# Optimization experiments

Measured on AMD Instinct MI355X. Metric: run time of the kernel, lower is better.

## Reference

```python
import jax, jax.numpy as jnp
import numpy as np

NUM_GROUPS = 5
EPS = 1e-5
QB = 128.0  # 2**(8-1) for b=8 activation quantization


def _binarize_weights_groupwise(W):
    """Sign-binarize W group-wise along out-feature dim, STE on backward.
    Faithful to torch: rows beyond num_groups*group_size remain zero."""
    n_out = W.shape[0]
    gs = n_out // NUM_GROUPS
    Wb = jnp.zeros_like(W)
    for g in range(NUM_GROUPS):  # small fixed loop (5 groups)
        wg = W[g * gs:(g + 1) * gs]
        z = wg - wg.mean()
        # STE: forward = sign(z), backward = identity w.r.t. z
        ste = z + jax.lax.stop_gradient(jnp.sign(z) - z)
        Wb = Wb.at[g * gs:(g + 1) * gs].set(ste)
    return Wb


def _quantize_activations_groupwise(x):
    """8-bit absmax quantization group-wise along dim 0 (batch), per torch code."""
    n = x.shape[0]
    gs = n // NUM_GROUPS
    xq = jnp.zeros_like(x)
    for g in range(NUM_GROUPS):
        ag = x[g * gs:(g + 1) * gs]
        gamma = jnp.max(jnp.abs(ag))
        xq = xq.at[g * gs:(g + 1) * gs].set(
            jnp.clip(ag * QB / (gamma + EPS), -QB + EPS, QB - EPS))
    return xq


def _bitlinear(x, W, b):
    Wb = _binarize_weights_groupwise(W)
    y = jnp.einsum('btc,oc->bto', x, Wb) + b
    return _quantize_activations_groupwise(y)


def setup_inputs() -> dict:
    key = jax.random.key(0)
    k1, k2, k3, k4, k5 = jax.random.split(key, 5)
    B, T, C = 10, 2048, 384
    H = 4 * C
    lim1 = 1.0 / np.sqrt(C)
    lim2 = 1.0 / np.sqrt(H)
    x = jax.random.normal(k1, (B, T, C), dtype=jnp.float32)
    W1 = jax.random.uniform(k2, (H, C), minval=-lim1, maxval=lim1, dtype=jnp.float32)
    b1 = jax.random.uniform(k3, (H,), minval=-lim1, maxval=lim1, dtype=jnp.float32)
    W2 = jax.random.uniform(k4, (C, H), minval=-lim2, maxval=lim2, dtype=jnp.float32)
    b2 = jax.random.uniform(k5, (C,), minval=-lim2, maxval=lim2, dtype=jnp.float32)
    return {"x": x, "W1": W1, "b1": b1, "W2": W2, "b2": b2}


def reference(x, W1, b1, W2, b2):
    h = _bitlinear(x, W1, b1)           # [B,T,4C], quantized to [-128,128]
    h = jax.nn.gelu(h, approximate=False)  # torch nn.GELU default is exact
    out = _bitlinear(h, W2, b2)         # [B,T,C]
    return out  # nn.Dropout is identity in eval/reference mode
```

## Files before the change

kernel.cpp:

```cpp
#include <hip/hip_runtime.h>
#include <cstdint>
#include <cstddef>

#define THREADS 256
#define NB 8

typedef float f32x4 __attribute__((ext_vector_type(4)));
typedef __bf16 bf16x8 __attribute__((ext_vector_type(8)));
typedef __bf16 bf16x4 __attribute__((ext_vector_type(4)));

__device__ __forceinline__ void gload_lds16(const void* g, void* l) {
    auto gp = (const __attribute__((address_space(1))) unsigned int*)(unsigned long long)(uintptr_t)g;
    auto lp = (__attribute__((address_space(3))) unsigned int*)(unsigned int)(uintptr_t)l;
    __builtin_amdgcn_global_load_lds(gp, lp, 16, 0, 0);
}

__device__ __forceinline__ float gelu_fast(float f) {
    const float z = f * 0.70710678118654752f;
    const float az = fabsf(z);
    const float t = __builtin_amdgcn_rcpf(fmaf(0.3275911f, az, 1.0f));
    float poly = fmaf(1.061405429f, t, -1.453152027f);
    poly = fmaf(poly, t, 1.421413741f);
    poly = fmaf(poly, t, -0.284496736f);
    poly = fmaf(poly, t, 0.254829592f);
    poly *= t;
    const float e = __builtin_amdgcn_exp2f(-az * az * 1.44269504088896f);
    float erfv = fmaf(-poly, e, 1.0f);
    erfv = copysignf(erfv, z);
    return 0.5f * f * (1.0f + erfv);
}

__global__ void prep_a(const float* __restrict__ x, __bf16* __restrict__ xb,
                       const float* __restrict__ W1, const float* __restrict__ W2,
                       float* __restrict__ partials, int epg1, int epg2,
                       unsigned int* __restrict__ gzero) {
    const int blk = blockIdx.x, tid = threadIdx.x;
    if (blk < 80) {
        const int y = blk >> 3, b = blk & 7;
        if (blk == 0 && tid < 16) gzero[tid] = 0u;
        const int epg = (y < 5) ? epg1 : epg2;
        const float* Wg = (y < 5) ? (W1 + (size_t)y * epg1)
                                  : (W2 + (size_t)(y - 5) * epg2);
        const int chunk4 = epg / (4 * NB);
        const float* base = Wg + (size_t)b * chunk4 * 4;
        float s = 0.f;
        for (int i = tid; i < chunk4; i += THREADS) {
            f32x4 v = *reinterpret_cast<const f32x4*>(base + 4 * (size_t)i);
            s += (v[0] + v[1]) + (v[2] + v[3]);
        }
        __shared__ float red[THREADS];
        red[tid] = s;
        __syncthreads();
        for (int off = THREADS / 2; off > 0; off >>= 1) {
            if (tid < off) red[tid] += red[tid + off];
            __syncthreads();
        }
        if (tid == 0) partials[y * NB + b] = red[0];
        return;
    }
    const int i = (blk - 80) * THREADS + tid;
    f32x4 v = *reinterpret_cast<const f32x4*>(x + 4 * (size_t)i);
    bf16x4 o;
    o[0] = (__bf16)v[0]; o[1] = (__bf16)v[1];
    o[2] = (__bf16)v[2]; o[3] = (__bf16)v[3];
    *reinterpret_cast<bf16x4*>(xb + 4 * (size_t)i) = o;
}

__global__ void prep_b(const float* __restrict__ W1, __bf16* __restrict__ W1b,
                       const float* __restrict__ W2, __bf16* __restrict__ W2b,
                       const float* __restrict__ psums,
                       int epg1, int tail1, int epg2, int tail2) {
    int r = blockIdx.x;
    const int tid = threadIdx.x;
    const float* W; __bf16* Wb; const float* ps; int epg, tail;
    if (r <= 40) { W = W1; Wb = W1b; ps = psums;      epg = epg1; tail = tail1; }
    else { r -= 41; W = W2; Wb = W2b; ps = psums + 40; epg = epg2; tail = tail2; }
    if (r == 40) {
        __bf16* og = Wb + (size_t)5 * epg;
        for (int i = tid; i < tail; i += THREADS) og[i] = (__bf16)0.f;
        return;
    }
    const int g = r >> 3, b = r & 7;
    float total = 0.f;
#pragma unroll
    for (int j = 0; j < NB; ++j) total += ps[g * NB + j];
    const float mean = total / (float)epg;
    const int chunk4 = epg / (4 * NB);
    const size_t off0 = (size_t)g * epg + (size_t)b * chunk4 * 4;
    const float* base = W + off0;
    __bf16* ob = Wb + off0;
    for (int i = tid; i < chunk4; i += THREADS) {
        f32x4 v = *reinterpret_cast<const f32x4*>(base + 4 * (size_t)i);
        bf16x4 o;
#pragma unroll
        for (int j = 0; j < 4; ++j) {
            const float z = v[j] - mean;
            o[j] = (__bf16)((z > 0.f) ? 1.f : ((z < 0.f) ? -1.f : 0.f));
        }
        *reinterpret_cast<bf16x4*>(ob + 4 * (size_t)i) = o;
    }
}

template<int OUT_BF16>
__global__ __launch_bounds__(512, 1)
void gemm_p3(const __bf16* __restrict__ A, const __bf16* __restrict__ Bw,
             const float* __restrict__ bias, void* __restrict__ outp,
             unsigned int* __restrict__ gmax, int M, int N, int K,
             int GN, int nwg) {
    constexpr int BM = 256, BN_ = 128, BK = 64, NF = 2;
    constexpr int ABYTES = BM * BK * 2;
    constexpr int BBYTES = BN_ * BK * 2;
    constexpr int BUF = ABYTES + BBYTES;
    __shared__ __attribute__((aligned(16))) char lds[3 * BUF];

    const int tid = threadIdx.x;
    const int wave = tid >> 6, lane = tid & 63;
    const int l15 = lane & 15, l4 = lane >> 4;
    const int wr = wave >> 2, wc = wave & 3;

    const int cpx = nwg >> 3;
    const int orig = (blockIdx.x & 7) * cpx + (blockIdx.x >> 3);
    const int bm = orig / GN, bn = orig % GN;

    const __bf16* Ab = A + (size_t)bm * BM * K;
    const __bf16* Bb = Bw + (size_t)bn * BN_ * K;
    const int NT = K / BK;

    f32x4 acc[8][NF];
#pragma unroll
    for (int m = 0; m < 8; ++m)
#pragma unroll
        for (int n = 0; n < NF; ++n)
            acc[m][n] = f32x4{0.f, 0.f, 0.f, 0.f};

    auto STAGE = [&](int t, int buf) {
        const int k0 = t * BK;
        char* ab = lds + buf * BUF;
        char* bb = ab + ABYTES;
#pragma unroll
        for (int j = 0; j < 4; ++j) {
            const int q = j * 8192 + tid * 16;
            const int lr = q >> 7;
            const int s = ((q >> 4) & 7) ^ (lr & 7);
            gload_lds16(Ab + (size_t)lr * K + k0 + s * 8, ab + q);
        }
#pragma unroll
        for (int j = 0; j < 2; ++j) {
            const int q = j * 8192 + tid * 16;
            const int lr = q >> 7;
            const int s = ((q >> 4) & 7) ^ (lr & 7);
            gload_lds16(Bb + (size_t)lr * K + k0 + s * 8, bb + q);
        }
    };

    STAGE(0, 0);
    STAGE(1, 1);
    asm volatile("s_waitcnt vmcnt(6)" ::: "memory");
    __syncthreads();

    int cur = 0;
    for (int t = 0; t < NT; ++t) {
        const int nxt2 = (cur >= 1) ? cur - 1 : cur + 2;
        if (t + 2 < NT) STAGE(t + 2, nxt2);
        const char* ab = lds + cur * BUF;
        const char* bb = ab + ABYTES;
#pragma unroll
        for (int kk = 0; kk < 2; ++kk) {
            bf16x8 af[8], bfv[NF];
#pragma unroll
            for (int m = 0; m < 8; ++m) {
                const int r = wr * 128 + m * 16 + l15;
                const int sp = (kk * 4 + l4) ^ (r & 7);
                af[m] = *reinterpret_cast<const bf16x8*>(ab + r * 128 + sp * 16);
            }
#pragma unroll
            for (int n = 0; n < NF; ++n) {
                const int r = wc * 32 + n * 16 + l15;
                const int sp = (kk * 4 + l4) ^ (r & 7);
                bfv[n] = *reinterpret_cast<const bf16x8*>(bb + r * 128 + sp * 16);
            }
#pragma unroll
            for (int m = 0; m < 8; ++m)
#pragma unroll
                for (int n = 0; n < NF; ++n)
                    acc[m][n] = __builtin_amdgcn_mfma_f32_16x16x32_bf16(
                        bfv[n], af[m], acc[m][n], 0, 0, 0);
        }
        if (t + 2 < NT)      asm volatile("s_waitcnt vmcnt(6)" ::: "memory");
        else if (t + 1 < NT) asm volatile("s_waitcnt vmcnt(0)" ::: "memory");
        __syncthreads();
        cur = (cur == 2) ? 0 : cur + 1;
    }

    const int rowb = bm * BM + wr * 128;
    const int colb = bn * BN_ + wc * 32;
    float lmax = 0.f;
#pragma unroll
    for (int n = 0; n < NF; ++n) {
        const f32x4 bv = *reinterpret_cast<const f32x4*>(bias + colb + n * 16 + l4 * 4);
#pragma unroll
        for (int m = 0; m < 8; ++m) {
            const int row = rowb + m * 16 + l15;
            if (OUT_BF16) {
                bf16x4 o;
#pragma unroll
                for (int r = 0; r < 4; ++r) {
                    const float v = acc[m][n][r] + bv[r];
                    lmax = fmaxf(lmax, fabsf(v));
                    o[r] = (__bf16)v;
                }
                *reinterpret_cast<bf16x4*>(
                    &((__bf16*)outp)[(size_t)row * N + colb + n * 16 + l4 * 4]) = o;
            } else {
                f32x4 o;
#pragma unroll
                for (int r = 0; r < 4; ++r) {
                    o[r] = acc[m][n][r] + bv[r];
                    lmax = fmaxf(lmax, fabsf(o[r]));
                }
                *reinterpret_cast<f32x4*>(
                    &((float*)outp)[(size_t)row * N + colb + n * 16 + l4 * 4]) = o;
            }
        }
    }
#pragma unroll
    for (int off = 32; off > 0; off >>= 1)
        lmax = fmaxf(lmax, __shfl_down(lmax, off, 64));
    float* wredmax = (float*)lds;
    if (lane == 0) wredmax[wave] = lmax;
    __syncthreads();
    if (tid == 0) {
        float bmax = wredmax[0];
#pragma unroll
        for (int w = 1; w < 8; ++w) bmax = fmaxf(bmax, wredmax[w]);
        atomicMax(gmax + (bm * BM) / 4096, __float_as_uint(bmax));
    }
}

__global__ void quant_gelu(__bf16* __restrict__ y, const unsigned int* __restrict__ gbits,
                           int perg8, int n8) {
    const int stride = gridDim.x * blockDim.x;
    for (int i = blockIdx.x * blockDim.x + threadIdx.x; i < n8; i += stride) {
        const int g = i / perg8;
        const float gamma = __uint_as_float(gbits[g]);
        const float s = 128.0f / (gamma + 1e-5f);
        bf16x8 v = *reinterpret_cast<const bf16x8*>(y + 8 * (size_t)i);
        bf16x8 o;
#pragma unroll
        for (int j = 0; j < 8; ++j) {
            float f = (float)v[j] * s;
            f = fminf(fmaxf(f, -128.0f + 1e-5f), 128.0f - 1e-5f);
            o[j] = (__bf16)gelu_fast(f);
        }
        *reinterpret_cast<bf16x8*>(y + 8 * (size_t)i) = o;
    }
}

__global__ void final_scale(float* __restrict__ y, const unsigned int* __restrict__ gbits,
                            int perg4, int n4) {
    int i = blockIdx.x * blockDim.x + threadIdx.x;
    if (i >= n4) return;
    const int g = i / perg4;
    const float gamma = __uint_as_float(gbits[g]);
    const float s = 128.0f / (gamma + 1e-5f);
    f32x4 v = *reinterpret_cast<const f32x4*>(y + 4 * (size_t)i);
    f32x4 o;
#pragma unroll
    for (int j = 0; j < 4; ++j)
        o[j] = fminf(fmaxf(v[j] * s, -128.0f + 1e-5f), 128.0f - 1e-5f);
    *reinterpret_cast<f32x4*>(y + 4 * (size_t)i) = o;
}

extern "C" void kernel_launch(void* const* d_in, const int* in_sizes, int n_in,
                              void* d_out, int out_size, void* d_ws, size_t ws_size,
                              hipStream_t stream) {
    const float* x  = (const float*)d_in[0];
    const float* W1 = (const float*)d_in[1];
    const float* b1 = (const float*)d_in[2];
    const float* W2 = (const float*)d_in[3];
    const float* b2 = (const float*)d_in[4];
    float* out = (float*)d_out;

    const int BB = 10, TT = 2048, C = 384, H = 1536;
    const int M = BB * TT;

    const int gs1 = H / 5;
    const int gs2 = C / 5;
    const int epg1 = gs1 * C;
    const int epg2 = gs2 * H;
    const int tail1 = (H - 5 * gs1) * C;
    const int tail2 = (C - 5 * gs2) * H;

    const size_t szW1b = (size_t)H * C * 2;
    const size_t szW2b = (size_t)C * H * 2;
    const size_t szXb  = (size_t)M * C * 2;
    const size_t szY1  = (size_t)M * H * 2;

    char* p = (char*)d_ws;
    __bf16* W1b = (__bf16*)p; p += szW1b;
    __bf16* W2b = (__bf16*)p; p += szW2b;
    __bf16* xb  = (__bf16*)p; p += szXb;
    __bf16* y1  = (__bf16*)p; p += szY1;
    unsigned int* gamma = (unsigned int*)p; p += 64;
    float* psums = (float*)p; p += 2 * 5 * NB * 4;
    if ((size_t)(p - (char*)d_ws) > ws_size) return;

    prep_a<<<7760, THREADS, 0, stream>>>(x, xb, W1, W2, psums, epg1, epg2, gamma);

    prep_b<<<82, THREADS, 0, stream>>>(W1, W1b, W2, W2b, psums,
                                       epg1, tail1, epg2, tail2);

    gemm_p3<1><<<960, 512, 0, stream>>>(
        xb, W1b, b1, (void*)y1, gamma, M, H, C, H / 128, 960);

    quant_gelu<<<2048, THREADS, 0, stream>>>(
        y1, gamma, (M / 5) * H / 8, M * H / 8);

    gemm_p3<0><<<240, 512, 0, stream>>>(
        y1, W2b, b2, (void*)out, gamma + 5, M, C, H, C / 128, 240);

    final_scale<<<(M * C / 4 + THREADS - 1) / THREADS, THREADS, 0, stream>>>(
        out, gamma + 5, (M / 5) * C / 4, M * C / 4);
}
```

Measured before the change: 139.0 us.

## Use 16-wave 1024-thread GEMM blocks with double-buffered LDS staging

Replaces the 8-wave 256x128 GEMM with a 16-wave (1024-thread) kernel templated on tile width. GEMM1 now uses 256x256 tiles, halving its block count, and GEMM2 keeps 256x128. Each wave holds a 64-row slice and fewer accumulators. The triple-buffered pipeline with partial vmcnt waits becomes a double buffer that waits for all loads every k-step. The aim is more waves per CU to hide latency, at the cost of exposing more load latency and fewer blocks for GEMM2's short grid.

```diff
diff --git a/kernel.cpp b/kernel.cpp
--- a/kernel.cpp
+++ b/kernel.cpp
@@ -101,17 +101,19 @@
     }
 }
 
-template<int OUT_BF16>
-__global__ __launch_bounds__(512, 1)
-void gemm_p3(const __bf16* __restrict__ A, const __bf16* __restrict__ Bw,
-             const float* __restrict__ bias, void* __restrict__ outp,
-             unsigned int* __restrict__ gmax, int M, int N, int K,
-             int GN, int nwg) {
-    constexpr int BM = 256, BN_ = 128, BK = 64, NF = 2;
+template<int BN_, int OUT_BF16>
+__global__ __launch_bounds__(1024, 1)
+void gemm_w16(const __bf16* __restrict__ A, const __bf16* __restrict__ Bw,
+              const float* __restrict__ bias, void* __restrict__ outp,
+              unsigned int* __restrict__ gmax, int M, int N, int K,
+              int GN, int nwg) {
+    constexpr int BM = 256, BK = 64;
+    constexpr int NF = BN_ / 64;
     constexpr int ABYTES = BM * BK * 2;
     constexpr int BBYTES = BN_ * BK * 2;
-    constexpr int BUF = ABYTES + BBYTES;
-    __shared__ __attribute__((aligned(16))) char lds[3 * BUF];
+    constexpr int AR = ABYTES / (1024 * 16);
+    constexpr int BR = BBYTES / (1024 * 16);
+    __shared__ __attribute__((aligned(16))) char lds[2 * (ABYTES + BBYTES)];
 
     const int tid = threadIdx.x;
     const int wave = tid >> 6, lane = tid & 63;
@@ -126,80 +128,75 @@
     const __bf16* Bb = Bw + (size_t)bn * BN_ * K;
     const int NT = K / BK;
 
-    f32x4 acc[8][NF];
-#pragma unroll
-    for (int m = 0; m < 8; ++m)
+    f32x4 acc[4][NF];
+#pragma unroll
+    for (int m = 0; m < 4; ++m)
 #pragma unroll
         for (int n = 0; n < NF; ++n)
             acc[m][n] = f32x4{0.f, 0.f, 0.f, 0.f};
 
-    auto STAGE = [&](int t, int buf) {
+    auto STAGE = [&](int t) {
         const int k0 = t * BK;
-        char* ab = lds + buf * BUF;
+        char* ab = lds + (t & 1) * (ABYTES + BBYTES);
         char* bb = ab + ABYTES;
 #pragma unroll
-        for (int j = 0; j < 4; ++j) {
-            const int q = j * 8192 + tid * 16;
+        for (int j = 0; j < AR; ++j) {
+            const int q = j * 16384 + tid * 16;
             const int lr = q >> 7;
             const int s = ((q >> 4) & 7) ^ (lr & 7);
             gload_lds16(Ab + (size_t)lr * K + k0 + s * 8, ab + q);
         }
 #pragma unroll
-        for (int j = 0; j < 2; ++j) {
-            const int q = j * 8192 + tid * 16;
+        for (int j = 0; j < BR; ++j) {
+            const int q = j * 16384 + tid * 16;
             const int lr = q >> 7;
             const int s = ((q >> 4) & 7) ^ (lr & 7);
             gload_lds16(Bb + (size_t)lr * K + k0 + s * 8, bb + q);
         }
     };
 
-    STAGE(0, 0);
-    STAGE(1, 1);
-    asm volatile("s_waitcnt vmcnt(6)" ::: "memory");
+    STAGE(0);
+    asm volatile("s_waitcnt vmcnt(0)" ::: "memory");
     __syncthreads();
 
-    int cur = 0;
     for (int t = 0; t < NT; ++t) {
-        const int nxt2 = (cur >= 1) ? cur - 1 : cur + 2;
-        if (t + 2 < NT) STAGE(t + 2, nxt2);
-        const char* ab = lds + cur * BUF;
+        if (t + 1 < NT) STAGE(t + 1);
+        const char* ab = lds + (t & 1) * (ABYTES + BBYTES);
         const char* bb = ab + ABYTES;
 #pragma unroll
         for (int kk = 0; kk < 2; ++kk) {
-            bf16x8 af[8], bfv[NF];
-#pragma unroll
-            for (int m = 0; m < 8; ++m) {
-                const int r = wr * 128 + m * 16 + l15;
+            bf16x8 af[4], bfv[NF];
+#pragma unroll
+            for (int m = 0; m < 4; ++m) {
+                const int r = wr * 64 + m * 16 + l15;
                 const int sp = (kk * 4 + l4) ^ (r & 7);
                 af[m] = *reinterpret_cast<const bf16x8*>(ab + r * 128 + sp * 16);
             }
 #pragma unroll
             for (int n = 0; n < NF; ++n) {
-                const int r = wc * 32 + n * 16 + l15;
+                const int r = wc * (BN_ / 4) + n * 16 + l15;
                 const int sp = (kk * 4 + l4) ^ (r & 7);
                 bfv[n] = *reinterpret_cast<const bf16x8*>(bb + r * 128 + sp * 16);
             }
 #pragma unroll
-            for (int m = 0; m < 8; ++m)
+            for (int m = 0; m < 4; ++m)
 #pragma unroll
                 for (int n = 0; n < NF; ++n)
                     acc[m][n] = __builtin_amdgcn_mfma_f32_16x16x32_bf16(
                         bfv[n], af[m], acc[m][n], 0, 0, 0);
         }
-        if (t + 2 < NT)      asm volatile("s_waitcnt vmcnt(6)" ::: "memory");
-        else if (t + 1 < NT) asm volatile("s_waitcnt vmcnt(0)" ::: "memory");
+        asm volatile("s_waitcnt vmcnt(0)" ::: "memory");
         __syncthreads();
-        cur = (cur == 2) ? 0 : cur + 1;
-    }
-
-    const int rowb = bm * BM + wr * 128;
-    const int colb = bn * BN_ + wc * 32;
+    }
+
+    const int rowb = bm * BM + wr * 64;
+    const int colb = bn * BN_ + wc * (BN_ / 4);
     float lmax = 0.f;
 #pragma unroll
     for (int n = 0; n < NF; ++n) {
         const f32x4 bv = *reinterpret_cast<const f32x4*>(bias + colb + n * 16 + l4 * 4);
 #pragma unroll
-        for (int m = 0; m < 8; ++m) {
+        for (int m = 0; m < 4; ++m) {
             const int row = rowb + m * 16 + l15;
             if (OUT_BF16) {
                 bf16x4 o;
@@ -232,7 +229,7 @@
     if (tid == 0) {
         float bmax = wredmax[0];
 #pragma unroll
-        for (int w = 1; w < 8; ++w) bmax = fmaxf(bmax, wredmax[w]);
+        for (int w = 1; w < 16; ++w) bmax = fmaxf(bmax, wredmax[w]);
         atomicMax(gmax + (bm * BM) / 4096, __float_as_uint(bmax));
     }
 }
@@ -310,13 +307,13 @@
     prep_b<<<82, THREADS, 0, stream>>>(W1, W1b, W2, W2b, psums,
                                        epg1, tail1, epg2, tail2);
 
-    gemm_p3<1><<<960, 512, 0, stream>>>(
-        xb, W1b, b1, (void*)y1, gamma, M, H, C, H / 128, 960);
+    gemm_w16<256, 1><<<480, 1024, 0, stream>>>(
+        xb, W1b, b1, (void*)y1, gamma, M, H, C, H / 256, 480);
 
     quant_gelu<<<2048, THREADS, 0, stream>>>(
         y1, gamma, (M / 5) * H / 8, M * H / 8);
 
-    gemm_p3<0><<<240, 512, 0, stream>>>(
+    gemm_w16<128, 0><<<240, 1024, 0, stream>>>(
         y1, W2b, b2, (void*)out, gamma + 5, M, C, H, C / 128, 240);
 
     final_scale<<<(M * C / 4 + THREADS - 1) / THREADS, THREADS, 0, stream>>>(
```

New measurement: 130.6 us (median of 2 runs). 6.0% less time.
